# Kernel optimization log

Hardware: AMD Instinct MI355X
Metric: run time of the kernel (lower is better)

## Reference

```python
import jax, jax.numpy as jnp
import numpy as np

D_MODEL = 1024
NHEAD = 16
HEAD_DIM = D_MODEL // NHEAD
D_FF = 4096
BIAS_HID = 8
EPS = 1e-5


def _pair_bias(m, w1, b1, w2, b2):
    # m: [B,S,S] -> bias [B,S,S,nhead] via per-scalar MLP 1->hid->nhead
    h = jax.nn.relu(m[..., None] * w1 + b1)          # [B,S,S,hid]
    return jnp.einsum('bxyh,hn->bxyn', h, w2) + b2   # [B,S,S,nhead]


def _layernorm(x, g, b):
    mu = jnp.mean(x, axis=-1, keepdims=True)
    var = jnp.mean(jnp.square(x - mu), axis=-1, keepdims=True)
    return (x - mu) * jax.lax.rsqrt(var + EPS) * g + b


def setup_inputs() -> dict:
    key = jax.random.key(0)
    ks = jax.random.split(key, 20)
    B, S = 4, 1024
    sc = 1.0 / np.sqrt(D_MODEL)
    inp = {
        'src': jax.random.normal(ks[0], (B, S, D_MODEL), jnp.float32),
        't_deltas': jax.random.uniform(ks[1], (B, S, S), jnp.float32),
        'dists': jax.random.uniform(ks[2], (B, S, S), jnp.float32),
        'Wq': jax.random.normal(ks[3], (D_MODEL, D_MODEL), jnp.float32) * sc,
        'bq': jnp.zeros((D_MODEL,), jnp.float32),
        'Wk': jax.random.normal(ks[4], (D_MODEL, D_MODEL), jnp.float32) * sc,
        'bk': jnp.zeros((D_MODEL,), jnp.float32),
        'Wv': jax.random.normal(ks[5], (D_MODEL, D_MODEL), jnp.float32) * sc,
        'bv': jnp.zeros((D_MODEL,), jnp.float32),
        'tb_w1': jax.random.normal(ks[6], (BIAS_HID,), jnp.float32),
        'tb_b1': jnp.zeros((BIAS_HID,), jnp.float32),
        'tb_w2': jax.random.normal(ks[7], (BIAS_HID, NHEAD), jnp.float32) * 0.3,
        'tb_b2': jnp.zeros((NHEAD,), jnp.float32),
        'db_w1': jax.random.normal(ks[8], (BIAS_HID,), jnp.float32),
        'db_b1': jnp.zeros((BIAS_HID,), jnp.float32),
        'db_w2': jax.random.normal(ks[9], (BIAS_HID, NHEAD), jnp.float32) * 0.3,
        'db_b2': jnp.zeros((NHEAD,), jnp.float32),
        'W1': jax.random.normal(ks[10], (D_MODEL, D_FF), jnp.float32) * sc,
        'b1': jnp.zeros((D_FF,), jnp.float32),
        'W2': jax.random.normal(ks[11], (D_FF, D_MODEL), jnp.float32) / np.sqrt(D_FF),
        'b2': jnp.zeros((D_MODEL,), jnp.float32),
        'g1': jnp.ones((D_MODEL,), jnp.float32),
        'beta1': jnp.zeros((D_MODEL,), jnp.float32),
        'g2': jnp.ones((D_MODEL,), jnp.float32),
        'beta2': jnp.zeros((D_MODEL,), jnp.float32),
    }
    return inp


def reference(src, t_deltas, dists, Wq, bq, Wk, bk, Wv, bv,
              tb_w1, tb_b1, tb_w2, tb_b2, db_w1, db_b1, db_w2, db_b2,
              W1, b1, W2, b2, g1, beta1, g2, beta2):
    B, S, _ = src.shape
    # QKV projections -> [B, H, S, hd]
    q = (src @ Wq + bq).reshape(B, S, NHEAD, HEAD_DIM).transpose(0, 2, 1, 3)
    k = (src @ Wk + bk).reshape(B, S, NHEAD, HEAD_DIM).transpose(0, 2, 1, 3)
    v = (src @ Wv + bv).reshape(B, S, NHEAD, HEAD_DIM).transpose(0, 2, 1, 3)
    # scores scaled by sqrt(d_model) (as in the original, not head_dim)
    scores = jnp.einsum('bhqd,bhkd->bhqk', q, k) / jnp.sqrt(jnp.float32(D_MODEL))
    bias = (_pair_bias(t_deltas, tb_w1, tb_b1, tb_w2, tb_b2)
            + _pair_bias(dists, db_w1, db_b1, db_w2, db_b2))  # [B,S,S,H]
    scores = scores + bias.transpose(0, 3, 1, 2)
    attn = jax.nn.softmax(scores, axis=-1)
    out = jnp.einsum('bhqk,bhkd->bhqd', attn, v)
    out = out.transpose(0, 2, 1, 3).reshape(B, S, D_MODEL)
    x = _layernorm(src + out, g1, beta1)
    ffn = jax.nn.relu(x @ W1 + b1) @ W2 + b2
    return _layernorm(x + ffn, g2, beta2)
```

## Files before the change

### kernel.cpp

```cpp
#include <hip/hip_runtime.h>

typedef __bf16 bf16x8 __attribute__((ext_vector_type(8)));
typedef float f32x4 __attribute__((ext_vector_type(4)));
typedef unsigned short u16;

__device__ __forceinline__ u16 f2bf(float f) {
  union { float f; unsigned u; } x; x.f = f;
  unsigned r = x.u + 0x7fffu + ((x.u >> 16) & 1u);
  return (u16)(r >> 16);
}
__device__ __forceinline__ float bf2f(u16 u) {
  union { unsigned u; float f; } x; x.u = ((unsigned)u) << 16;
  return x.f;
}
__device__ __forceinline__ void gl_lds16(const void* g, void* l) {
  __builtin_amdgcn_global_load_lds(
      (const __attribute__((address_space(1))) void*)g,
      (__attribute__((address_space(3))) void*)l, 16, 0, 0);
}

__global__ __launch_bounds__(256) void cvt_kernel(const float* __restrict__ in,
                                                  u16* __restrict__ out, int n4) {
  int i = blockIdx.x * 256 + threadIdx.x;
  if (i >= n4) return;
  float4 v = ((const float4*)in)[i];
  unsigned lo = (unsigned)f2bf(v.x) | ((unsigned)f2bf(v.y) << 16);
  unsigned hi = (unsigned)f2bf(v.z) | ((unsigned)f2bf(v.w) << 16);
  uint2 u; u.x = lo; u.y = hi;
  *(uint2*)&out[(size_t)i * 4] = u;
}

__global__ __launch_bounds__(256) void tconv_kernel(const float* __restrict__ in,
                                                    u16* __restrict__ out, int R, int C) {
  __shared__ float tile[32][33];
  int c0 = blockIdx.x * 32, r0 = blockIdx.y * 32;
  int tx = threadIdx.x & 31, ty = threadIdx.x >> 5;
#pragma unroll
  for (int i = 0; i < 4; i++)
    tile[ty + i * 8][tx] = in[(size_t)(r0 + ty + i * 8) * C + c0 + tx];
  __syncthreads();
#pragma unroll
  for (int i = 0; i < 4; i++)
    out[(size_t)(c0 + ty + i * 8) * R + r0 + tx] = f2bf(tile[tx][ty + i * 8]);
}

__global__ __launch_bounds__(256) void bcat_kernel(const float* __restrict__ bq,
                                                   const float* __restrict__ bk,
                                                   const float* __restrict__ bv,
                                                   float* __restrict__ o) {
  int i = blockIdx.x * 256 + threadIdx.x;
  if (i >= 3072) return;
  o[i] = i < 1024 ? bq[i] : (i < 2048 ? bk[i - 1024] : bv[i - 2048]);
}

__device__ __forceinline__ void stage256(u16* ldsA, u16* ldsB,
                                         const u16* Ag, const u16* Bg,
                                         int K, int w, int lane) {
  int r8 = lane >> 3;
  int gcol = 8 * ((lane & 7) ^ r8);
#pragma unroll
  for (int c = 0; c < 4; c++) {
    int r = c * 64 + w * 8 + r8;
    gl_lds16(Ag + (size_t)r * K + gcol, ldsA + c * 4096 + w * 512);
    gl_lds16(Bg + (size_t)r * K + gcol, ldsB + c * 4096 + w * 512);
  }
}

template <int EPI>
__global__ __launch_bounds__(512, 2) void gemm256_kernel(const u16* __restrict__ A,
                                                         const u16* __restrict__ Bt,
                                                         const float* __restrict__ bias,
                                                         void* __restrict__ out,
                                                         int M, int N, int K,
                                                         float qscale, int kslice) {
  __shared__ u16 lds[2][2][16384];
  int tid = threadIdx.x, w = tid >> 6, lane = tid & 63;
  int l16 = lane & 15, lhi = lane >> 4;
  int wr = w >> 2, wc = w & 3;
  int GX = gridDim.x;
  int nwg = GX * gridDim.y;
  int nlin = blockIdx.y * GX + blockIdx.x;
  int cpx = nwg >> 3;
  int sw = (nlin & 7) * cpx + (nlin >> 3);
  int m0 = (sw / GX) * 256, n0 = (sw % GX) * 256;
  int z = blockIdx.z;
  int kbeg = z * kslice;
  const u16* Ag = A + (size_t)m0 * K + kbeg;
  const u16* Bg = Bt + (size_t)n0 * K + kbeg;
  f32x4 acc[8][4] = {};
  int colq0 = ((lhi) ^ (l16 & 7)) << 3;
  int colq1 = ((4 | lhi) ^ (l16 & 7)) << 3;
  int nt = kslice >> 6;

  stage256(&lds[0][0][0], &lds[0][1][0], Ag, Bg, K, w, lane);
  stage256(&lds[1][0][0], &lds[1][1][0], Ag + 64, Bg + 64, K, w, lane);

  for (int t = 0; t < nt; ++t) {
    if (t + 1 < nt) { asm volatile("s_waitcnt vmcnt(8)" ::: "memory"); }
    else            { asm volatile("s_waitcnt vmcnt(0)" ::: "memory"); }
    __builtin_amdgcn_s_barrier();
    const u16* Ab = &lds[t & 1][0][0];
    const u16* Bb = &lds[t & 1][1][0];
#pragma unroll
    for (int kk = 0; kk < 2; kk++) {
      int cq = kk ? colq1 : colq0;
      bf16x8 af[8], bfr[4];
#pragma unroll
      for (int m = 0; m < 8; m++)
        af[m] = *(const bf16x8*)&Ab[(wr * 128 + m * 16 + l16) * 64 + cq];
#pragma unroll
      for (int nn = 0; nn < 4; nn++)
        bfr[nn] = *(const bf16x8*)&Bb[(wc * 64 + nn * 16 + l16) * 64 + cq];
      __builtin_amdgcn_s_setprio(1);
#pragma unroll
      for (int m = 0; m < 8; m++)
#pragma unroll
        for (int nn = 0; nn < 4; nn++)
          acc[m][nn] = __builtin_amdgcn_mfma_f32_16x16x32_bf16(af[m], bfr[nn], acc[m][nn], 0, 0, 0);
      __builtin_amdgcn_s_setprio(0);
    }
    __builtin_amdgcn_s_barrier();
    if (t + 2 < nt)
      stage256(&lds[t & 1][0][0], &lds[t & 1][1][0],
               Ag + (t + 2) * 64, Bg + (t + 2) * 64, K, w, lane);
  }

#pragma unroll
  for (int m = 0; m < 8; m++) {
    int gr = m0 + wr * 128 + m * 16 + lhi * 4;
#pragma unroll
    for (int nn = 0; nn < 4; nn++) {
      int gc = n0 + wc * 64 + nn * 16 + l16;
      float bv;
      if (EPI == 0 || EPI == 3) bv = (z == 0 && bias) ? bias[gc] : 0.f;
      else bv = bias[gc];
      if (EPI == 2) {
        int seg = gc >> 10, c = gc & 1023, h = c >> 6, d = c & 63;
        float sc = (seg == 0) ? qscale : 1.f;
#pragma unroll
        for (int r = 0; r < 4; r++) {
          int row = gr + r;
          int b = row >> 10, s = row & 1023;
          size_t idx = ((((size_t)seg * 4 + b) * 16 + h) * 1024 + s) * 64 + d;
          ((u16*)out)[idx] = f2bf((acc[m][nn][r] + bv) * sc);
        }
      } else if (EPI == 1) {
#pragma unroll
        for (int r = 0; r < 4; r++)
          ((u16*)out)[(size_t)(gr + r) * N + gc] = f2bf(fmaxf(acc[m][nn][r] + bv, 0.f));
      } else if (EPI == 3) {
#pragma unroll
        for (int r = 0; r < 4; r++)
          ((u16*)out)[(size_t)z * M * N + (size_t)(gr + r) * N + gc] = f2bf(acc[m][nn][r] + bv);
      } else {
#pragma unroll
        for (int r = 0; r < 4; r++)
          ((float*)out)[(size_t)z * M * N + (size_t)(gr + r) * N + gc] = acc[m][nn][r] + bv;
      }
    }
  }
}

__global__ __launch_bounds__(256) void vtrans_kernel(const u16* __restrict__ v,
                                                     u16* __restrict__ vt) {
  __shared__ u16 t[64][72];
  int bh = blockIdx.y, s0 = blockIdx.x * 64;
  int tid = threadIdx.x;
  int r = tid >> 2, c = (tid & 3) * 16;
  const u16* src = v + ((size_t)bh * 1024 + s0 + r) * 64 + c;
  *(int4*)&t[r][c] = *(const int4*)src;
  *(int4*)&t[r][c + 8] = *(const int4*)(src + 8);
  __syncthreads();
  int d = tid >> 2, sc = (tid & 3) * 16;
  u16 tmp[16];
#pragma unroll
  for (int j = 0; j < 16; j++) tmp[j] = t[sc + j][d];
  u16* dst = vt + ((size_t)bh * 64 + d) * 1024 + s0 + sc;
  *(int4*)dst = *(int4*)&tmp[0];
  *(int4*)(dst + 8) = *(int4*)&tmp[8];
}

__global__ __launch_bounds__(256) void bias_kernel(
    const float* __restrict__ td, const float* __restrict__ dd,
    const float* __restrict__ tw1, const float* __restrict__ tb1,
    const float* __restrict__ tw2, const float* __restrict__ tb2,
    const float* __restrict__ dw1, const float* __restrict__ db1,
    const float* __restrict__ dw2, const float* __restrict__ db2,
    u16* __restrict__ biasout, int b0) {
  __shared__ float stw2[128], sdw2[128], sb2[16];
  __shared__ float stw1[8], stb1[8], sdw1[8], sdb1[8];
  int tid = threadIdx.x, x = blockIdx.x, bz = blockIdx.y;
  int b = b0 + bz;
  if (tid < 128) { stw2[tid] = tw2[tid]; sdw2[tid] = dw2[tid]; }
  if (tid < 16) sb2[tid] = tb2[tid] + db2[tid];
  if (tid < 8) { stw1[tid] = tw1[tid]; stb1[tid] = tb1[tid]; sdw1[tid] = dw1[tid]; sdb1[tid] = db1[tid]; }
  __syncthreads();
  float4 tv = ((const float4*)(td + ((size_t)b * 1024 + x) * 1024))[tid];
  float4 dv = ((const float4*)(dd + ((size_t)b * 1024 + x) * 1024))[tid];
  float tj[4] = {tv.x, tv.y, tv.z, tv.w};
  float dj[4] = {dv.x, dv.y, dv.z, dv.w};
  float ht[4][8], hd[4][8];
#pragma unroll
  for (int j = 0; j < 4; j++)
#pragma unroll
    for (int i = 0; i < 8; i++) {
      ht[j][i] = fmaxf(tj[j] * stw1[i] + stb1[i], 0.f);
      hd[j][i] = fmaxf(dj[j] * sdw1[i] + sdb1[i], 0.f);
    }
  u16* outb = biasout + (size_t)bz * 16 * 1024 * 1024 + (size_t)x * 1024 + tid * 4;
#pragma unroll
  for (int h = 0; h < 16; h++) {
    float a[4];
#pragma unroll
    for (int j = 0; j < 4; j++) {
      float s = sb2[h];
#pragma unroll
      for (int i = 0; i < 8; i++)
        s += ht[j][i] * stw2[i * 16 + h] + hd[j][i] * sdw2[i * 16 + h];
      a[j] = s;
    }
    unsigned lo = (unsigned)f2bf(a[0]) | ((unsigned)f2bf(a[1]) << 16);
    unsigned hi = (unsigned)f2bf(a[2]) | ((unsigned)f2bf(a[3]) << 16);
    uint2 u; u.x = lo; u.y = hi;
    *(uint2*)&outb[(size_t)h * 1024 * 1024] = u;
  }
}

#define LDA 72
__global__ __launch_bounds__(256) void attn_kernel(
    const u16* __restrict__ qg, const u16* __restrict__ kg, const u16* __restrict__ vtg,
    const u16* __restrict__ bias, float* __restrict__ attn_out, int b0) {
  __shared__ u16 Ks[64 * LDA];
  __shared__ u16 Vt[64 * LDA];
  __shared__ u16 Ps[64 * LDA];
  int tid = threadIdx.x;
  int w = tid >> 6, l = tid & 63, l16 = l & 15, lhi = l >> 4;
  int qt = blockIdx.x, h = blockIdx.y, bz = blockIdx.z;
  int b = b0 + bz;
  size_t bh = ((size_t)(b * 16 + h)) * 1024 * 64;
  const u16* biasb = bias + (size_t)bz * 16 * 1024 * 1024 + (size_t)h * 1024 * 1024;
  int qrow = qt * 64 + w * 16 + l16;
  bf16x8 qa[2];
  qa[0] = *(const bf16x8*)&qg[bh + (size_t)qrow * 64 + lhi * 8];
  qa[1] = *(const bf16x8*)&qg[bh + (size_t)qrow * 64 + 32 + lhi * 8];

  float m_run[4], l_run[4];
  f32x4 o[4] = {};
#pragma unroll
  for (int r = 0; r < 4; r++) { m_run[r] = -1e30f; l_run[r] = 0.f; }

  int kr0 = (tid * 2) >> 3, kc0 = ((tid * 2) & 7) * 8;
  int kr1 = (tid * 2 + 1) >> 3, kc1 = ((tid * 2 + 1) & 7) * 8;

  for (int kt = 0; kt < 16; kt++) {
    __syncthreads();
    *(int4*)&Ks[kr0 * LDA + kc0] = *(const int4*)&kg[bh + (size_t)(kt * 64 + kr0) * 64 + kc0];
    *(int4*)&Ks[kr1 * LDA + kc1] = *(const int4*)&kg[bh + (size_t)(kt * 64 + kr1) * 64 + kc1];
    *(int4*)&Vt[kr0 * LDA + kc0] = *(const int4*)&vtg[bh + (size_t)kr0 * 1024 + kt * 64 + kc0];
    *(int4*)&Vt[kr1 * LDA + kc1] = *(const int4*)&vtg[bh + (size_t)kr1 * 1024 + kt * 64 + kc1];
    __syncthreads();

    f32x4 s[4] = {};
    __builtin_amdgcn_s_setprio(1);
#pragma unroll
    for (int ni = 0; ni < 4; ni++)
#pragma unroll
      for (int ks = 0; ks < 2; ks++) {
        bf16x8 kb = *(const bf16x8*)&Ks[(ni * 16 + l16) * LDA + ks * 32 + lhi * 8];
        s[ni] = __builtin_amdgcn_mfma_f32_16x16x32_bf16(qa[ks], kb, s[ni], 0, 0, 0);
      }
    __builtin_amdgcn_s_setprio(0);
#pragma unroll
    for (int ni = 0; ni < 4; ni++)
#pragma unroll
      for (int r = 0; r < 4; r++) {
        int brow = qt * 64 + w * 16 + lhi * 4 + r;
        s[ni][r] += bf2f(biasb[(size_t)brow * 1024 + kt * 64 + ni * 16 + l16]);
      }
    float rs[4];
#pragma unroll
    for (int r = 0; r < 4; r++) {
      float m = fmaxf(fmaxf(s[0][r], s[1][r]), fmaxf(s[2][r], s[3][r]));
      m = fmaxf(m, __shfl_xor(m, 1, 16));
      m = fmaxf(m, __shfl_xor(m, 2, 16));
      m = fmaxf(m, __shfl_xor(m, 4, 16));
      m = fmaxf(m, __shfl_xor(m, 8, 16));
      float m2 = fmaxf(m_run[r], m);
      float sc = __expf(m_run[r] - m2);
      float sum = 0.f;
#pragma unroll
      for (int ni = 0; ni < 4; ni++) {
        float p = __expf(s[ni][r] - m2);
        s[ni][r] = p;
        sum += p;
      }
      sum += __shfl_xor(sum, 1, 16);
      sum += __shfl_xor(sum, 2, 16);
      sum += __shfl_xor(sum, 4, 16);
      sum += __shfl_xor(sum, 8, 16);
      l_run[r] = l_run[r] * sc + sum;
      m_run[r] = m2;
      rs[r] = sc;
    }
#pragma unroll
    for (int di = 0; di < 4; di++)
#pragma unroll
      for (int r = 0; r < 4; r++)
        o[di][r] *= rs[r];
#pragma unroll
    for (int ni = 0; ni < 4; ni++)
#pragma unroll
      for (int r = 0; r < 4; r++)
        Ps[(w * 16 + lhi * 4 + r) * LDA + ni * 16 + l16] = f2bf(s[ni][r]);
    __builtin_amdgcn_s_setprio(1);
#pragma unroll
    for (int ks = 0; ks < 2; ks++) {
      bf16x8 pa = *(const bf16x8*)&Ps[(w * 16 + l16) * LDA + ks * 32 + lhi * 8];
#pragma unroll
      for (int di = 0; di < 4; di++) {
        bf16x8 vb = *(const bf16x8*)&Vt[(di * 16 + l16) * LDA + ks * 32 + lhi * 8];
        o[di] = __builtin_amdgcn_mfma_f32_16x16x32_bf16(pa, vb, o[di], 0, 0, 0);
      }
    }
    __builtin_amdgcn_s_setprio(0);
  }
#pragma unroll
  for (int r = 0; r < 4; r++) {
    float inv = 1.f / l_run[r];
    int row = b * 1024 + qt * 64 + w * 16 + lhi * 4 + r;
#pragma unroll
    for (int di = 0; di < 4; di++)
      attn_out[(size_t)row * 1024 + h * 64 + di * 16 + l16] = o[di][r] * inv;
  }
}

__global__ __launch_bounds__(256) void ln_kernel(const float* __restrict__ a,
                                                 const float* __restrict__ r1,
                                                 const float* __restrict__ g,
                                                 const float* __restrict__ beta,
                                                 float* __restrict__ outf,
                                                 u16* __restrict__ outbf) {
  int row = blockIdx.x, tid = threadIdx.x;
  __shared__ float red[8];
  float4 va = ((const float4*)(a + (size_t)row * 1024))[tid];
  float4 vr = ((const float4*)(r1 + (size_t)row * 1024))[tid];
  float v[4] = {va.x + vr.x, va.y + vr.y, va.z + vr.z, va.w + vr.w};
  float s = v[0] + v[1] + v[2] + v[3];
#pragma unroll
  for (int off = 32; off >= 1; off >>= 1) s += __shfl_xor(s, off, 64);
  if ((tid & 63) == 0) red[tid >> 6] = s;
  __syncthreads();
  float mean = (red[0] + red[1] + red[2] + red[3]) * (1.f / 1024.f);
  float q = 0.f;
#pragma unroll
  for (int j = 0; j < 4; j++) { float d = v[j] - mean; q += d * d; }
#pragma unroll
  for (int off = 32; off >= 1; off >>= 1) q += __shfl_xor(q, off, 64);
  if ((tid & 63) == 0) red[4 + (tid >> 6)] = q;
  __syncthreads();
  float var = (red[4] + red[5] + red[6] + red[7]) * (1.f / 1024.f);
  float rstd = rsqrtf(var + 1e-5f);
  float4 gv = ((const float4*)g)[tid];
  float4 bv = ((const float4*)beta)[tid];
  float o0 = (v[0] - mean) * rstd * gv.x + bv.x;
  float o1 = (v[1] - mean) * rstd * gv.y + bv.y;
  float o2 = (v[2] - mean) * rstd * gv.z + bv.z;
  float o3 = (v[3] - mean) * rstd * gv.w + bv.w;
  float4 ov; ov.x = o0; ov.y = o1; ov.z = o2; ov.w = o3;
  ((float4*)(outf + (size_t)row * 1024))[tid] = ov;
  unsigned lo = (unsigned)f2bf(o0) | ((unsigned)f2bf(o1) << 16);
  unsigned hi = (unsigned)f2bf(o2) | ((unsigned)f2bf(o3) << 16);
  uint2 u; u.x = lo; u.y = hi;
  *(uint2*)&outbf[(size_t)row * 1024 + tid * 4] = u;
}

__global__ __launch_bounds__(256) void ln2_kernel(const float* __restrict__ x,
                                                  const u16* __restrict__ ff, int zs,
                                                  const float* __restrict__ g,
                                                  const float* __restrict__ beta,
                                                  float* __restrict__ out) {
  int row = blockIdx.x, tid = threadIdx.x;
  __shared__ float red[8];
  float4 xv = ((const float4*)(x + (size_t)row * 1024))[tid];
  float v[4] = {xv.x, xv.y, xv.z, xv.w};
  for (int z = 0; z < zs; z++) {
    uint2 u = *(const uint2*)&ff[(size_t)z * 4096 * 1024 + (size_t)row * 1024 + tid * 4];
    v[0] += bf2f(u.x & 0xffff); v[1] += bf2f(u.x >> 16);
    v[2] += bf2f(u.y & 0xffff); v[3] += bf2f(u.y >> 16);
  }
  float s = v[0] + v[1] + v[2] + v[3];
#pragma unroll
  for (int off = 32; off >= 1; off >>= 1) s += __shfl_xor(s, off, 64);
  if ((tid & 63) == 0) red[tid >> 6] = s;
  __syncthreads();
  float mean = (red[0] + red[1] + red[2] + red[3]) * (1.f / 1024.f);
  float q = 0.f;
#pragma unroll
  for (int j = 0; j < 4; j++) { float d = v[j] - mean; q += d * d; }
#pragma unroll
  for (int off = 32; off >= 1; off >>= 1) q += __shfl_xor(q, off, 64);
  if ((tid & 63) == 0) red[4 + (tid >> 6)] = q;
  __syncthreads();
  float var = (red[4] + red[5] + red[6] + red[7]) * (1.f / 1024.f);
  float rstd = rsqrtf(var + 1e-5f);
  float4 gv = ((const float4*)g)[tid];
  float4 bv = ((const float4*)beta)[tid];
  float4 ov;
  ov.x = (v[0] - mean) * rstd * gv.x + bv.x;
  ov.y = (v[1] - mean) * rstd * gv.y + bv.y;
  ov.z = (v[2] - mean) * rstd * gv.z + bv.z;
  ov.w = (v[3] - mean) * rstd * gv.w + bv.w;
  ((float4*)(out + (size_t)row * 1024))[tid] = ov;
}

extern "C" void kernel_launch(void* const* d_in, const int* in_sizes, int n_in,
                              void* d_out, int out_size, void* d_ws, size_t ws_size,
                              hipStream_t stream) {
  const float* src      = (const float*)d_in[0];
  const float* t_deltas = (const float*)d_in[1];
  const float* dists    = (const float*)d_in[2];
  const float* Wq = (const float*)d_in[3];
  const float* bq = (const float*)d_in[4];
  const float* Wk = (const float*)d_in[5];
  const float* bk = (const float*)d_in[6];
  const float* Wv = (const float*)d_in[7];
  const float* bv = (const float*)d_in[8];
  const float* tb_w1 = (const float*)d_in[9];
  const float* tb_b1 = (const float*)d_in[10];
  const float* tb_w2 = (const float*)d_in[11];
  const float* tb_b2 = (const float*)d_in[12];
  const float* db_w1 = (const float*)d_in[13];
  const float* db_b1 = (const float*)d_in[14];
  const float* db_w2 = (const float*)d_in[15];
  const float* db_b2 = (const float*)d_in[16];
  const float* W1 = (const float*)d_in[17];
  const float* b1 = (const float*)d_in[18];
  const float* W2 = (const float*)d_in[19];
  const float* b2 = (const float*)d_in[20];
  const float* g1 = (const float*)d_in[21];
  const float* beta1 = (const float*)d_in[22];
  const float* g2 = (const float*)d_in[23];
  const float* beta2 = (const float*)d_in[24];
  float* out = (float*)d_out;

  const size_t MB = 1024u * 1024;
  bool big = ws_size >= 150 * MB;
  int PB = big ? 2 : 1;
  int ZS = big ? 4 : 2;

  char* ws = (char*)d_ws;
  size_t off = 0;
  auto alloc = [&](size_t n) { void* p = ws + off; off += (n + 255) & ~(size_t)255; return p; };
  u16* src_bf  = (u16*)alloc(4096u * 1024 * 2);
  u16* wqkv_bt = (u16*)alloc(3072u * 1024 * 2);
  u16* w1_bt   = (u16*)alloc(4096u * 1024 * 2);
  u16* w2_bt   = (u16*)alloc(1024u * 4096 * 2);
  float* bcat  = (float*)alloc(3072u * 4);
  u16* qkv     = (u16*)alloc(3u * 4 * 16 * 1024 * 64 * 2);
  u16* vt      = (u16*)alloc(4u * 16 * 64 * 1024 * 2);
  u16* slab    = (u16*)alloc((size_t)PB * 16 * 1024 * 1024 * 2);
  float* attn_out = (float*)alloc(4096u * 1024 * 4);
  (void)in_sizes; (void)n_in; (void)out_size;

  u16* q_bf = qkv;
  u16* k_bf = qkv + 4u * 16 * 1024 * 64;
  u16* v_bf = qkv + 8u * 16 * 1024 * 64;
  float* x_f32 = (float*)qkv;
  u16*   x_bf  = (u16*)((char*)qkv + 16 * MB);
  u16*   h_bf  = (u16*)vt;
  u16*   ffnb  = big ? (u16*)((char*)slab + 24 * MB)
                     : (u16*)attn_out;

  cvt_kernel<<<4096, 256, 0, stream>>>(src, src_bf, 4096 * 1024 / 4);
  tconv_kernel<<<dim3(32, 32), 256, 0, stream>>>(Wq, wqkv_bt, 1024, 1024);
  tconv_kernel<<<dim3(32, 32), 256, 0, stream>>>(Wk, wqkv_bt + 1024u * 1024, 1024, 1024);
  tconv_kernel<<<dim3(32, 32), 256, 0, stream>>>(Wv, wqkv_bt + 2048u * 1024, 1024, 1024);
  tconv_kernel<<<dim3(128, 32), 256, 0, stream>>>(W1, w1_bt, 1024, 4096);
  tconv_kernel<<<dim3(32, 128), 256, 0, stream>>>(W2, w2_bt, 4096, 1024);
  bcat_kernel<<<12, 256, 0, stream>>>(bq, bk, bv, bcat);

  gemm256_kernel<2><<<dim3(12, 16, 1), 512, 0, stream>>>(src_bf, wqkv_bt, bcat, qkv,
                                                         4096, 3072, 1024, 1.f / 32.f, 1024);
  vtrans_kernel<<<dim3(16, 64), 256, 0, stream>>>(v_bf, vt);

  for (int p = 0; p < 4 / PB; p++) {
    bias_kernel<<<dim3(1024, PB), 256, 0, stream>>>(t_deltas, dists, tb_w1, tb_b1, tb_w2, tb_b2,
                                                    db_w1, db_b1, db_w2, db_b2, slab, p * PB);
    attn_kernel<<<dim3(16, 16, PB), 256, 0, stream>>>(q_bf, k_bf, vt, slab, attn_out, p * PB);
  }

  ln_kernel<<<4096, 256, 0, stream>>>(src, attn_out, g1, beta1, x_f32, x_bf);
  gemm256_kernel<1><<<dim3(16, 16, 1), 512, 0, stream>>>(x_bf, w1_bt, b1, h_bf,
                                                         4096, 4096, 1024, 1.f, 1024);
  gemm256_kernel<3><<<dim3(4, 16, ZS), 512, 0, stream>>>(h_bf, w2_bt, b2, ffnb,
                                                         4096, 1024, 4096, 1.f, 4096 / ZS);
  ln2_kernel<<<4096, 256, 0, stream>>>(x_f32, ffnb, ZS, g2, beta2, out);
}
```

Baseline: 299.1 us.

## Interleave half-tile LDS staging with MFMA in 256x256 GEMM main loop

After: 300.6 us. No clear change (+0.5%).

```diff
diff --git a/kernel.cpp b/kernel.cpp
--- a/kernel.cpp
+++ b/kernel.cpp
@@ -51,19 +51,6 @@
   int i = blockIdx.x * 256 + threadIdx.x;
   if (i >= 3072) return;
   o[i] = i < 1024 ? bq[i] : (i < 2048 ? bk[i - 1024] : bv[i - 2048]);
-}
-
-__device__ __forceinline__ void stage256(u16* ldsA, u16* ldsB,
-                                         const u16* Ag, const u16* Bg,
-                                         int K, int w, int lane) {
-  int r8 = lane >> 3;
-  int gcol = 8 * ((lane & 7) ^ r8);
-#pragma unroll
-  for (int c = 0; c < 4; c++) {
-    int r = c * 64 + w * 8 + r8;
-    gl_lds16(Ag + (size_t)r * K + gcol, ldsA + c * 4096 + w * 512);
-    gl_lds16(Bg + (size_t)r * K + gcol, ldsB + c * 4096 + w * 512);
-  }
 }
 
 template <int EPI>
@@ -84,50 +71,83 @@
   int sw = (nlin & 7) * cpx + (nlin >> 3);
   int m0 = (sw / GX) * 256, n0 = (sw % GX) * 256;
   int z = blockIdx.z;
-  int kbeg = z * kslice;
-  const u16* Ag = A + (size_t)m0 * K + kbeg;
-  const u16* Bg = Bt + (size_t)n0 * K + kbeg;
+  const u16* Ag = A + (size_t)m0 * K + z * kslice;
+  const u16* Bg = Bt + (size_t)n0 * K + z * kslice;
   f32x4 acc[8][4] = {};
-  int colq0 = ((lhi) ^ (l16 & 7)) << 3;
-  int colq1 = ((4 | lhi) ^ (l16 & 7)) << 3;
+  const int c0q = (lhi ^ (l16 & 7)) << 3;
+  const int c1q = ((4 | lhi) ^ (l16 & 7)) << 3;
   int nt = kslice >> 6;
-
-  stage256(&lds[0][0][0], &lds[0][1][0], Ag, Bg, K, w, lane);
-  stage256(&lds[1][0][0], &lds[1][1][0], Ag + 64, Bg + 64, K, w, lane);
+  int r8 = lane >> 3;
+  int gcol = 8 * ((lane & 7) ^ r8);
+
+  auto stageHalf = [&](int p, int ab, int half, const u16* G) {
+#pragma unroll
+    for (int i = 0; i < 2; i++) {
+      int r = half * 128 + i * 64 + w * 8 + r8;
+      gl_lds16(G + (size_t)r * K + gcol,
+               &lds[p][ab][(half * 128 + i * 64 + w * 8) * 64]);
+    }
+  };
+  auto rdA = [&](int p, int mh, int cq, bf16x8* af) {
+#pragma unroll
+    for (int j = 0; j < 4; j++)
+      af[j] = *(const bf16x8*)&lds[p][0][(mh * 128 + wr * 64 + j * 16 + l16) * 64 + cq];
+  };
+  auto rdB = [&](int p, int cq, bf16x8* bfr) {
+#pragma unroll
+    for (int nn = 0; nn < 4; nn++)
+      bfr[nn] = *(const bf16x8*)&lds[p][1][(wc * 64 + nn * 16 + l16) * 64 + cq];
+  };
+  auto mma = [&](int mh, bf16x8* af, bf16x8* bfr) {
+    __builtin_amdgcn_s_setprio(1);
+#pragma unroll
+    for (int j = 0; j < 4; j++)
+#pragma unroll
+      for (int nn = 0; nn < 4; nn++)
+        acc[mh * 4 + j][nn] =
+            __builtin_amdgcn_mfma_f32_16x16x32_bf16(af[j], bfr[nn], acc[mh * 4 + j][nn], 0, 0, 0);
+    __builtin_amdgcn_s_setprio(0);
+  };
+
+  stageHalf(0, 1, 0, Bg);
+  stageHalf(0, 0, 0, Ag);
+  stageHalf(0, 1, 1, Bg);
+  stageHalf(0, 0, 1, Ag);
+  asm volatile("s_waitcnt vmcnt(2)" ::: "memory");
+  __builtin_amdgcn_s_barrier();
 
   for (int t = 0; t < nt; ++t) {
-    if (t + 1 < nt) { asm volatile("s_waitcnt vmcnt(8)" ::: "memory"); }
-    else            { asm volatile("s_waitcnt vmcnt(0)" ::: "memory"); }
+    int p = t & 1, pn = p ^ 1;
+    const u16* An = Ag + (t + 1) * 64;
+    const u16* Bn = Bg + (t + 1) * 64;
+    bool more = (t + 1 < nt);
+    bf16x8 af[4], bfr[4];
+    rdA(p, 0, c0q, af); rdB(p, c0q, bfr);
+    if (more) { stageHalf(pn, 1, 0, Bn); stageHalf(pn, 0, 0, An); }
+    mma(0, af, bfr);
+    rdA(p, 0, c1q, af); rdB(p, c1q, bfr);
+    if (more) {
+      stageHalf(pn, 1, 1, Bn);
+      asm volatile("s_waitcnt vmcnt(6)" ::: "memory");
+    } else {
+      asm volatile("s_waitcnt vmcnt(0)" ::: "memory");
+    }
     __builtin_amdgcn_s_barrier();
-    const u16* Ab = &lds[t & 1][0][0];
-    const u16* Bb = &lds[t & 1][1][0];
-#pragma unroll
-    for (int kk = 0; kk < 2; kk++) {
-      int cq = kk ? colq1 : colq0;
-      bf16x8 af[8], bfr[4];
-#pragma unroll
-      for (int m = 0; m < 8; m++)
-        af[m] = *(const bf16x8*)&Ab[(wr * 128 + m * 16 + l16) * 64 + cq];
-#pragma unroll
-      for (int nn = 0; nn < 4; nn++)
-        bfr[nn] = *(const bf16x8*)&Bb[(wc * 64 + nn * 16 + l16) * 64 + cq];
-      __builtin_amdgcn_s_setprio(1);
-#pragma unroll
-      for (int m = 0; m < 8; m++)
-#pragma unroll
-        for (int nn = 0; nn < 4; nn++)
-          acc[m][nn] = __builtin_amdgcn_mfma_f32_16x16x32_bf16(af[m], bfr[nn], acc[m][nn], 0, 0, 0);
-      __builtin_amdgcn_s_setprio(0);
-    }
-    __builtin_amdgcn_s_barrier();
-    if (t + 2 < nt)
-      stage256(&lds[t & 1][0][0], &lds[t & 1][1][0],
-               Ag + (t + 2) * 64, Bg + (t + 2) * 64, K, w, lane);
+    mma(0, af, bfr);
+    rdA(p, 1, c0q, af); rdB(p, c0q, bfr);
+    mma(1, af, bfr);
+    rdA(p, 1, c1q, af); rdB(p, c1q, bfr);
+    if (more) stageHalf(pn, 0, 1, An);
+    mma(1, af, bfr);
+    if (more) {
+      asm volatile("s_waitcnt vmcnt(2)" ::: "memory");
+      __builtin_amdgcn_s_barrier();
+    }
   }
 
 #pragma unroll
   for (int m = 0; m < 8; m++) {
-    int gr = m0 + wr * 128 + m * 16 + lhi * 4;
+    int gr = m0 + (m >> 2) * 128 + wr * 64 + (m & 3) * 16 + lhi * 4;
 #pragma unroll
     for (int nn = 0; nn < 4; nn++) {
       int gc = n0 + wc * 64 + nn * 16 + l16;
```
